# Optimization experiments

Measured on AMD Instinct MI355X. Metric: run time of the kernel, lower is better.

The kernel has to match this reference:

```python
import jax, jax.numpy as jnp
import numpy as np

B, N, H = 8, 1024, 1024
HEADS, DH = 16, 64  # H = HEADS * DH
LN_EPS = 1e-12


def setup_inputs() -> dict:
    key = jax.random.key(0)
    ks = jax.random.split(key, 8)
    s = 0.02
    return {
        "hidden_states": jax.random.normal(ks[0], (B, N, H), jnp.float32),
        "role_mask": jax.random.randint(ks[1], (B, N, N), 0, 2, jnp.int32),
        "conv_len": jax.random.randint(ks[2], (B,), 0, 160, jnp.int32),
        "Wq": jax.random.normal(ks[3], (H, H), jnp.float32) * s,
        "bq": jnp.zeros((H,), jnp.float32),
        "Wk": jax.random.normal(ks[4], (H, H), jnp.float32) * s,
        "bk": jnp.zeros((H,), jnp.float32),
        "Wv": jax.random.normal(ks[5], (H, H), jnp.float32) * s,
        "bv": jnp.zeros((H,), jnp.float32),
        "Wo": jax.random.normal(ks[6], (H, H), jnp.float32) * s,
        "bo": jnp.zeros((H,), jnp.float32),
        "gamma": jnp.ones((H,), jnp.float32),
        "beta": jnp.zeros((H,), jnp.float32),
    }


def _split_heads(x):
    b, n, h = x.shape
    return x.reshape(b, n, HEADS, DH).transpose(0, 2, 1, 3)  # [B,h,N,dh]


def reference(hidden_states, role_mask, conv_len, Wq, bq, Wk, bk, Wv, bv, Wo, bo, gamma, beta):
    q = _split_heads(hidden_states @ Wq + bq)
    k = _split_heads(hidden_states @ Wk + bk)
    v = _split_heads(hidden_states @ Wv + bv)

    scale = 1.0 / jnp.sqrt(jnp.asarray(DH, hidden_states.dtype))
    scores = jnp.einsum("bhqd,bhkd->bhqk", q, k) * scale  # [B,h,N,N]
    scores = jnp.where(role_mask[:, None, :, :] == 0, jnp.asarray(-1e9, scores.dtype), scores)
    probs = jax.nn.softmax(scores, axis=-1)  # dropout is identity in eval

    ctx = jnp.einsum("bhqk,bhkd->bhqd", probs, v)
    ctx = ctx.transpose(0, 2, 1, 3).reshape(hidden_states.shape)  # [B,N,H]

    # output projection + residual + LayerNorm (BERT-style, eps=1e-12)
    y = ctx @ Wo + bo + hidden_states
    mu = jnp.mean(y, axis=-1, keepdims=True)
    var = jnp.mean(jnp.square(y - mu), axis=-1, keepdims=True)
    context_layer = (y - mu) / jnp.sqrt(var + LN_EPS) * gamma + beta

    # state_type == 'user': rows 6*idx+2 (perspective) and 6*idx+3 (emotion)
    bidx = jnp.arange(context_layer.shape[0])
    base = 6 * conv_len
    perspective_taking = context_layer[bidx, base + 2]  # [B,H]
    high_emo_states = context_layer[bidx, base + 3]     # [B,H]
    return context_layer, high_emo_states, perspective_taking
```

## Files before the change

### kernel.cpp

```cpp
#include <hip/hip_runtime.h>
#include <math.h>

#define HN 1024
#define BB 8
#define NN 1024
#define NHEADS 16
#define DH 64
#define M_ROWS (BB * NN)

typedef __attribute__((ext_vector_type(8))) short short8;
typedef __attribute__((ext_vector_type(8))) unsigned short ushort8v;
typedef __attribute__((ext_vector_type(4))) float floatx4;

__device__ __forceinline__ unsigned short f2bf(float f) {
    unsigned int u = __builtin_bit_cast(unsigned int, f);
    u += 0x7fffu + ((u >> 16) & 1u);
    return (unsigned short)(u >> 16);
}

__device__ __forceinline__ void gload16(const unsigned short* g, unsigned short* l) {
    __builtin_amdgcn_global_load_lds(
        (const __attribute__((address_space(1))) void*)g,
        (__attribute__((address_space(3))) void*)l, 16, 0, 0);
}

__global__ __launch_bounds__(256)
void cvt_hs_k(const float* __restrict__ in, unsigned short* __restrict__ out)
{
    int i = (blockIdx.x * 256 + threadIdx.x) * 4;
    float4 v = *(const float4*)(in + i);
    ushort4 o;
    o.x = f2bf(v.x); o.y = f2bf(v.y); o.z = f2bf(v.z); o.w = f2bf(v.w);
    *(ushort4*)&out[i] = o;
}

__global__ __launch_bounds__(256)
void cvt_wT4_k(const float* __restrict__ W0, const float* __restrict__ W1,
               const float* __restrict__ W2, const float* __restrict__ W3,
               unsigned short* __restrict__ o0, unsigned short* __restrict__ o1,
               unsigned short* __restrict__ o2, unsigned short* __restrict__ o3)
{
    __shared__ float Ls[32][33];
    const int z = blockIdx.z;
    const float* W = z == 0 ? W0 : (z == 1 ? W1 : (z == 2 ? W2 : W3));
    unsigned short* out = z == 0 ? o0 : (z == 1 ? o1 : (z == 2 ? o2 : o3));
    const int t = threadIdx.x;
    const int k0 = blockIdx.x * 32, n0 = blockIdx.y * 32;
    const int r = t >> 3, c4 = (t & 7) * 4;
    float4 v = *(const float4*)(W + (size_t)(k0 + r) * HN + n0 + c4);
    Ls[r][c4 + 0] = v.x; Ls[r][c4 + 1] = v.y;
    Ls[r][c4 + 2] = v.z; Ls[r][c4 + 3] = v.w;
    __syncthreads();
    ushort4 o;
    o.x = f2bf(Ls[c4 + 0][r]); o.y = f2bf(Ls[c4 + 1][r]);
    o.z = f2bf(Ls[c4 + 2][r]); o.w = f2bf(Ls[c4 + 3][r]);
    *(ushort4*)&out[(size_t)(n0 + r) * HN + k0 + c4] = o;
}

__global__ __launch_bounds__(256)
void mfma_gemm_k(const unsigned short* __restrict__ A,
                 const unsigned short* __restrict__ Bt,
                 const float* __restrict__ b0p, const float* __restrict__ b1p,
                 const float* __restrict__ b2p,
                 const float* __restrict__ resid,
                 unsigned short* __restrict__ Qb, unsigned short* __restrict__ Kb,
                 unsigned short* __restrict__ Vtb, float* __restrict__ Yb,
                 int mode)
{
    __shared__ unsigned short smem[128 * 136];
    unsigned short* As = smem;
    unsigned short* Bs = smem + 4096;

    const int tid  = threadIdx.x;
    const int wave = tid >> 6, lane = tid & 63;
    const int quad = lane >> 4, n16 = lane & 15;
    const int wm = wave >> 1, wn = wave & 1;
    const int row0 = blockIdx.y * 128;
    const int n0   = blockIdx.x * 128;

    floatx4 acc[4][4];
    #pragma unroll
    for (int mi = 0; mi < 4; ++mi)
        #pragma unroll
        for (int ni = 0; ni < 4; ++ni)
            acc[mi][ni] = (floatx4){0.f, 0.f, 0.f, 0.f};

    const unsigned short* ga = A  + (size_t)(row0 + wave * 32 + (lane >> 2)) * 1024 + (lane & 3) * 8;
    const unsigned short* gb = Bt + (size_t)(n0  + wave * 32 + (lane >> 2)) * 1024 + (lane & 3) * 8;

    for (int k0 = 0; k0 < 1024; k0 += 32) {
        gload16(ga,             As + wave * 1024);
        gload16(ga + 16 * 1024, As + wave * 1024 + 512);
        gload16(gb,             Bs + wave * 1024);
        gload16(gb + 16 * 1024, Bs + wave * 1024 + 512);
        ga += 32; gb += 32;
        __syncthreads();

        short8 a[4], b[4];
        #pragma unroll
        for (int mi = 0; mi < 4; ++mi)
            a[mi] = *(const short8*)&As[(wm * 64 + mi * 16 + n16) * 32 + quad * 8];
        #pragma unroll
        for (int ni = 0; ni < 4; ++ni)
            b[ni] = *(const short8*)&Bs[(wn * 64 + ni * 16 + n16) * 32 + quad * 8];
        #pragma unroll
        for (int mi = 0; mi < 4; ++mi)
            #pragma unroll
            for (int ni = 0; ni < 4; ++ni)
                acc[mi][ni] = __builtin_amdgcn_mfma_f32_16x16x32_bf16(
                    a[mi], b[ni], acc[mi][ni], 0, 0, 0);
        __syncthreads();
    }

    if (mode == 0) {
        const int sel = n0 >> 10;
        const int c0  = n0 & 1023;
        const float* bias = sel == 0 ? b0p : (sel == 1 ? b1p : b2p);
        float bvv[4];
        #pragma unroll
        for (int ni = 0; ni < 4; ++ni)
            bvv[ni] = bias[c0 + wn * 64 + ni * 16 + n16];

        #pragma unroll
        for (int mi = 0; mi < 4; ++mi)
            #pragma unroll
            for (int ni = 0; ni < 4; ++ni)
                #pragma unroll
                for (int r = 0; r < 4; ++r)
                    smem[(wm * 64 + mi * 16 + quad * 4 + r) * 136 +
                         wn * 64 + ni * 16 + n16] = f2bf(acc[mi][ni][r] + bvv[ni]);
        __syncthreads();

        if (sel < 2) {
            unsigned short* outb = sel == 0 ? Qb : Kb;
            #pragma unroll
            for (int i = 0; i < 8; ++i) {
                int c = i * 256 + tid;
                int r = c >> 4;
                int colc = (c & 15) * 8;
                ushort8v v = *(const ushort8v*)&smem[r * 136 + colc];
                int row = row0 + r, bb = row >> 10, nn = row & 1023;
                int gc = c0 + colc, head = gc >> 6, d = gc & 63;
                *(ushort8v*)&outb[(((size_t)bb * NHEADS + head) * NN + nn) * DH + d] = v;
            }
        } else {
            #pragma unroll
            for (int i = 0; i < 8; ++i) {
                int c = i * 256 + tid;
                int dcol = c >> 4;
                int nnc = (c & 15) * 8;
                ushort8v v;
                #pragma unroll
                for (int j = 0; j < 8; ++j)
                    v[j] = smem[(nnc + j) * 136 + dcol];
                int gc = c0 + dcol, head = gc >> 6, d = gc & 63;
                int row = row0 + nnc, bb = row >> 10, nn = row & 1023;
                *(ushort8v*)&Vtb[(((size_t)bb * NHEADS + head) * DH + d) * NN + nn] = v;
            }
        }
    } else {
        float bvv[4];
        #pragma unroll
        for (int ni = 0; ni < 4; ++ni)
            bvv[ni] = b0p[n0 + wn * 64 + ni * 16 + n16];
        #pragma unroll
        for (int mi = 0; mi < 4; ++mi)
            #pragma unroll
            for (int r = 0; r < 4; ++r) {
                int row = row0 + wm * 64 + mi * 16 + quad * 4 + r;
                const float* rr = resid + (size_t)row * HN;
                float* yr = Yb + (size_t)row * HN;
                #pragma unroll
                for (int ni = 0; ni < 4; ++ni) {
                    int col = n0 + wn * 64 + ni * 16 + n16;
                    yr[col] = acc[mi][ni][r] + bvv[ni] + rr[col];
                }
            }
    }
}

__global__ __launch_bounds__(256)
void attn_mfma_k(const unsigned short* __restrict__ Q,
                 const unsigned short* __restrict__ K,
                 const unsigned short* __restrict__ Vt,
                 const int* __restrict__ mask,
                 unsigned short* __restrict__ ctx)
{
    __shared__ unsigned short Ks[64][72];
    __shared__ unsigned short Vs[64][72];
    __shared__ unsigned short Ps[4][16][72];

    const int tid  = threadIdx.x;
    const int wave = tid >> 6, lane = tid & 63;
    const int quad = lane >> 4, n16 = lane & 15;
    const int q0 = blockIdx.x << 6;
    const int h  = blockIdx.y, b = blockIdx.z;
    const int bh = b * NHEADS + h;
    const int qw = q0 + wave * 16;
    const float SC = 0.125f * 1.44269504088896340736f;

    const unsigned short* qp = Q + ((size_t)bh * NN + qw + n16) * DH;
    short8 aq0 = *(const short8*)(qp + quad * 8);
    short8 aq1 = *(const short8*)(qp + 32 + quad * 8);

    floatx4 O[4];
    #pragma unroll
    for (int d4 = 0; d4 < 4; ++d4) O[d4] = (floatx4){0.f, 0.f, 0.f, 0.f};
    float lsum = 0.f;

    const unsigned short* Kg = K  + (size_t)bh * NN * DH;
    const unsigned short* Vg = Vt + (size_t)bh * DH * NN;
    const int srow = tid >> 2;
    const int scol = (tid & 3) << 4;
    const int* mp = mask + ((size_t)b * NN + qw + n16) * NN + quad * 4;

    for (int k0 = 0; k0 < NN; k0 += 64) {
        __syncthreads();
        {
            const unsigned short* ks = Kg + (size_t)(k0 + srow) * DH + scol;
            *(ushort8v*)&Ks[srow][scol]     = *(const ushort8v*)(ks);
            *(ushort8v*)&Ks[srow][scol + 8] = *(const ushort8v*)(ks + 8);
            const unsigned short* vs = Vg + (size_t)srow * NN + k0 + scol;
            *(ushort8v*)&Vs[srow][scol]     = *(const ushort8v*)(vs);
            *(ushort8v*)&Vs[srow][scol + 8] = *(const ushort8v*)(vs + 8);
        }
        __syncthreads();

        #pragma unroll
        for (int kt = 0; kt < 4; ++kt) {
            short8 kf0 = *(const short8*)&Ks[kt * 16 + n16][quad * 8];
            short8 kf1 = *(const short8*)&Ks[kt * 16 + n16][32 + quad * 8];
            floatx4 s = (floatx4){0.f, 0.f, 0.f, 0.f};
            s = __builtin_amdgcn_mfma_f32_16x16x32_bf16(kf0, aq0, s, 0, 0, 0);
            s = __builtin_amdgcn_mfma_f32_16x16x32_bf16(kf1, aq1, s, 0, 0, 0);

            int4 m4 = *(const int4*)(mp + k0 + kt * 16);
            float p0 = m4.x ? exp2f(s[0] * SC) : 0.f;
            float p1 = m4.y ? exp2f(s[1] * SC) : 0.f;
            float p2 = m4.z ? exp2f(s[2] * SC) : 0.f;
            float p3 = m4.w ? exp2f(s[3] * SC) : 0.f;
            lsum += (p0 + p1) + (p2 + p3);
            ushort4 pk;
            pk.x = f2bf(p0); pk.y = f2bf(p1); pk.z = f2bf(p2); pk.w = f2bf(p3);
            *(ushort4*)&Ps[wave][n16][kt * 16 + quad * 4] = pk;
        }

        #pragma unroll
        for (int c = 0; c < 2; ++c) {
            short8 pa = *(const short8*)&Ps[wave][n16][c * 32 + quad * 8];
            #pragma unroll
            for (int d4 = 0; d4 < 4; ++d4) {
                short8 vb = *(const short8*)&Vs[d4 * 16 + n16][c * 32 + quad * 8];
                O[d4] = __builtin_amdgcn_mfma_f32_16x16x32_bf16(pa, vb, O[d4], 0, 0, 0);
            }
        }
    }

    float ltot = lsum;
    ltot += __shfl_xor(ltot, 16);
    ltot += __shfl_xor(ltot, 32);
    float inv[4];
    #pragma unroll
    for (int r = 0; r < 4; ++r)
        inv[r] = 1.0f / __shfl(ltot, quad * 4 + r);

    unsigned short* cp = ctx + ((size_t)b * NN + qw + quad * 4) * HN + h * DH + n16;
    #pragma unroll
    for (int d4 = 0; d4 < 4; ++d4)
        #pragma unroll
        for (int r = 0; r < 4; ++r)
            cp[(size_t)r * HN + d4 * 16] = f2bf(O[d4][r] * inv[r]);
}

__global__ __launch_bounds__(256)
void ln_ext_k(const float* __restrict__ y, const float* __restrict__ gamma,
              const float* __restrict__ beta, const int* __restrict__ conv_len,
              float* __restrict__ out, float* __restrict__ he, float* __restrict__ pt)
{
    const int row = blockIdx.x;
    const int t = threadIdx.x;
    float4 v = ((const float4*)(y + (size_t)row * HN))[t];
    float s  = v.x + v.y + v.z + v.w;
    float s2 = v.x * v.x + v.y * v.y + v.z * v.z + v.w * v.w;
    #pragma unroll
    for (int off = 32; off > 0; off >>= 1) {
        s  += __shfl_down(s, off);
        s2 += __shfl_down(s2, off);
    }
    __shared__ float ws1[4], ws2[4];
    __shared__ float smu, sinv;
    if ((t & 63) == 0) { ws1[t >> 6] = s; ws2[t >> 6] = s2; }
    __syncthreads();
    if (t == 0) {
        float ts  = ws1[0] + ws1[1] + ws1[2] + ws1[3];
        float ts2 = ws2[0] + ws2[1] + ws2[2] + ws2[3];
        float mu  = ts * (1.0f / 1024.0f);
        float var = ts2 * (1.0f / 1024.0f) - mu * mu;
        smu  = mu;
        sinv = 1.0f / sqrtf(var + 1e-12f);
    }
    __syncthreads();
    const float mu = smu, inv = sinv;
    float4 g = ((const float4*)gamma)[t];
    float4 be = ((const float4*)beta)[t];
    float4 o;
    o.x = (v.x - mu) * inv * g.x + be.x;
    o.y = (v.y - mu) * inv * g.y + be.y;
    o.z = (v.z - mu) * inv * g.z + be.z;
    o.w = (v.w - mu) * inv * g.w + be.w;
    ((float4*)(out + (size_t)row * HN))[t] = o;

    const int b = row >> 10, n = row & 1023;
    const int base = 6 * conv_len[b];
    if (n == base + 3) ((float4*)(he + (size_t)b * HN))[t] = o;
    if (n == base + 2) ((float4*)(pt + (size_t)b * HN))[t] = o;
}

extern "C" void kernel_launch(void* const* d_in, const int* in_sizes, int n_in,
                              void* d_out, int out_size, void* d_ws, size_t ws_size,
                              hipStream_t stream)
{
    const float* hs    = (const float*)d_in[0];
    const int*   mask  = (const int*)d_in[1];
    const int*   clen  = (const int*)d_in[2];
    const float* Wq    = (const float*)d_in[3];
    const float* bq    = (const float*)d_in[4];
    const float* Wk    = (const float*)d_in[5];
    const float* bk    = (const float*)d_in[6];
    const float* Wv    = (const float*)d_in[7];
    const float* bv    = (const float*)d_in[8];
    const float* Wo    = (const float*)d_in[9];
    const float* bo    = (const float*)d_in[10];
    const float* gamma = (const float*)d_in[11];
    const float* beta  = (const float*)d_in[12];
    float* out = (float*)d_out;

    unsigned short* Ab  = (unsigned short*)d_ws;
    unsigned short* Wt3 = Ab  + (size_t)M_ROWS * HN;
    unsigned short* Wot = Wt3 + (size_t)3 * HN * HN;
    unsigned short* Qb  = Wot + (size_t)HN * HN;
    unsigned short* Kb  = Qb  + (size_t)M_ROWS * HN;
    unsigned short* Vtb = Kb  + (size_t)M_ROWS * HN;
    unsigned short* Ctx = Vtb + (size_t)M_ROWS * HN;
    float*          Yb  = (float*)Qb;

    dim3 gb(256);

    hipLaunchKernelGGL(cvt_hs_k, dim3((size_t)M_ROWS * HN / 1024), gb, 0, stream, hs, Ab);
    hipLaunchKernelGGL(cvt_wT4_k, dim3(32, 32, 4), gb, 0, stream,
                       Wq, Wk, Wv, Wo,
                       Wt3, Wt3 + (size_t)HN * HN, Wt3 + (size_t)2 * HN * HN, Wot);

    hipLaunchKernelGGL(mfma_gemm_k, dim3(24, 64), gb, 0, stream,
                       Ab, Wt3, bq, bk, bv, (const float*)nullptr,
                       Qb, Kb, Vtb, (float*)nullptr, 0);

    hipLaunchKernelGGL(attn_mfma_k, dim3(NN / 64, NHEADS, BB), gb, 0, stream,
                       Qb, Kb, Vtb, mask, Ctx);

    hipLaunchKernelGGL(mfma_gemm_k, dim3(8, 64), gb, 0, stream,
                       Ctx, Wot, bo, (const float*)nullptr, (const float*)nullptr, hs,
                       (unsigned short*)nullptr, (unsigned short*)nullptr,
                       (unsigned short*)nullptr, Yb, 1);

    float* he = out + (size_t)BB * NN * HN;
    float* pt = he + BB * HN;
    hipLaunchKernelGGL(ln_ext_k, dim3(M_ROWS), gb, 0, stream, Yb, gamma, beta, clen,
                       out, he, pt);
}
```

Baseline: 388.4 us.

## Double-buffer K/V tiles via direct global-to-LDS loads with XOR swizzle

The attention kernel now uses two LDS buffers for K and V. The next 64-key tile is prefetched with global_load_lds while the current tile is consumed, so one barrier per iteration replaces the synchronous copy and its two barriers. Padded LDS arrays are replaced by unpadded 64-wide rows with an XOR column swizzle for K, V and P, to avoid bank conflicts without padding. The main risk is correctness of the asynchronous LDS writes: it depends on the compiler placing the vmcnt waits before the barrier. LDS use also grows with the second buffer.

New measurement: 384.9 us. About the same (-0.9%).

```diff
diff --git a/kernel.cpp b/kernel.cpp
--- a/kernel.cpp
+++ b/kernel.cpp
@@ -186,13 +186,14 @@
                  const int* __restrict__ mask,
                  unsigned short* __restrict__ ctx)
 {
-    __shared__ unsigned short Ks[64][72];
-    __shared__ unsigned short Vs[64][72];
-    __shared__ unsigned short Ps[4][16][72];
+    __shared__ unsigned short KsB[2 * 4096];
+    __shared__ unsigned short VsB[2 * 4096];
+    __shared__ unsigned short PsB[4 * 1024];
 
     const int tid  = threadIdx.x;
     const int wave = tid >> 6, lane = tid & 63;
     const int quad = lane >> 4, n16 = lane & 15;
+    const int sw   = n16 & 7;
     const int q0 = blockIdx.x << 6;
     const int h  = blockIdx.y, b = blockIdx.z;
     const int bh = b * NHEADS + h;
@@ -210,31 +211,44 @@
 
     const unsigned short* Kg = K  + (size_t)bh * NN * DH;
     const unsigned short* Vg = Vt + (size_t)bh * DH * NN;
-    const int srow = tid >> 2;
-    const int scol = (tid & 3) << 4;
+
+    const int r8 = lane >> 3, cs = (lane & 7) ^ r8;
+    const unsigned short* kg0 = Kg + (size_t)(wave * 16 + r8) * DH + cs * 8;
+    const unsigned short* kg1 = kg0 + 8 * DH;
+    const unsigned short* vg0 = Vg + (size_t)(wave * 16 + r8) * NN + cs * 8;
+    const unsigned short* vg1 = vg0 + 8 * NN;
+    unsigned short* lk = KsB + wave * 1024;
+    unsigned short* lv = VsB + wave * 1024;
+    unsigned short* Pw = PsB + wave * 1024;
+
     const int* mp = mask + ((size_t)b * NN + qw + n16) * NN + quad * 4;
 
-    for (int k0 = 0; k0 < NN; k0 += 64) {
+    gload16(kg0, lk);       gload16(kg1, lk + 512);
+    gload16(vg0, lv);       gload16(vg1, lv + 512);
+
+    for (int t = 0; t < 16; ++t) {
         __syncthreads();
-        {
-            const unsigned short* ks = Kg + (size_t)(k0 + srow) * DH + scol;
-            *(ushort8v*)&Ks[srow][scol]     = *(const ushort8v*)(ks);
-            *(ushort8v*)&Ks[srow][scol + 8] = *(const ushort8v*)(ks + 8);
-            const unsigned short* vs = Vg + (size_t)srow * NN + k0 + scol;
-            *(ushort8v*)&Vs[srow][scol]     = *(const ushort8v*)(vs);
-            *(ushort8v*)&Vs[srow][scol + 8] = *(const ushort8v*)(vs + 8);
+        const int cur = t & 1;
+        if (t < 15) {
+            const int nxt = cur ^ 1;
+            kg0 += 4096; kg1 += 4096; vg0 += 64; vg1 += 64;
+            gload16(kg0, lk + nxt * 4096); gload16(kg1, lk + nxt * 4096 + 512);
+            gload16(vg0, lv + nxt * 4096); gload16(vg1, lv + nxt * 4096 + 512);
         }
-        __syncthreads();
+        const unsigned short* Kc = KsB + cur * 4096;
+        const unsigned short* Vc = VsB + cur * 4096;
+        const int kbase = t * 64;
 
         #pragma unroll
         for (int kt = 0; kt < 4; ++kt) {
-            short8 kf0 = *(const short8*)&Ks[kt * 16 + n16][quad * 8];
-            short8 kf1 = *(const short8*)&Ks[kt * 16 + n16][32 + quad * 8];
+            const unsigned short* kr = Kc + (kt * 16 + n16) * 64;
+            short8 kf0 = *(const short8*)&kr[(quad ^ sw) * 8];
+            short8 kf1 = *(const short8*)&kr[((quad + 4) ^ sw) * 8];
             floatx4 s = (floatx4){0.f, 0.f, 0.f, 0.f};
             s = __builtin_amdgcn_mfma_f32_16x16x32_bf16(kf0, aq0, s, 0, 0, 0);
             s = __builtin_amdgcn_mfma_f32_16x16x32_bf16(kf1, aq1, s, 0, 0, 0);
 
-            int4 m4 = *(const int4*)(mp + k0 + kt * 16);
+            int4 m4 = *(const int4*)(mp + kbase + kt * 16);
             float p0 = m4.x ? exp2f(s[0] * SC) : 0.f;
             float p1 = m4.y ? exp2f(s[1] * SC) : 0.f;
             float p2 = m4.z ? exp2f(s[2] * SC) : 0.f;
@@ -242,15 +256,17 @@
             lsum += (p0 + p1) + (p2 + p3);
             ushort4 pk;
             pk.x = f2bf(p0); pk.y = f2bf(p1); pk.z = f2bf(p2); pk.w = f2bf(p3);
-            *(ushort4*)&Ps[wave][n16][kt * 16 + quad * 4] = pk;
+            *(ushort4*)&Pw[n16 * 64 + ((2 * kt + (quad >> 1)) ^ sw) * 8 +
+                           (quad & 1) * 4] = pk;
         }
 
         #pragma unroll
         for (int c = 0; c < 2; ++c) {
-            short8 pa = *(const short8*)&Ps[wave][n16][c * 32 + quad * 8];
+            const int cc = ((c << 2) + quad) ^ sw;
+            short8 pa = *(const short8*)&Pw[n16 * 64 + cc * 8];
             #pragma unroll
             for (int d4 = 0; d4 < 4; ++d4) {
-                short8 vb = *(const short8*)&Vs[d4 * 16 + n16][c * 32 + quad * 8];
+                short8 vb = *(const short8*)&Vc[(d4 * 16 + n16) * 64 + cc * 8];
                 O[d4] = __builtin_amdgcn_mfma_f32_16x16x32_bf16(pa, vb, O[d4], 0, 0, 0);
             }
         }
```
